# Optimization experiments

Measured on AMD Instinct MI355X. Metric: run time of the kernel, lower is better.

## Reference

```python
import jax, jax.numpy as jnp
import numpy as np

N_NODES = 50000
N_EDGES = 800000
IN_DIM = 128
HID = 64
HEADS = 4
OUT_DIM = 64
NEG_SLOPE = 0.2


def setup_inputs() -> dict:
    key = jax.random.key(0)
    ks = jax.random.split(key, 12)
    x = jax.random.normal(ks[0], (N_NODES, IN_DIM), dtype=jnp.float32)
    edge_index = jax.random.randint(ks[1], (2, N_EDGES), 0, N_NODES, dtype=jnp.int64)
    s = 0.1
    # GATConv layer 1: in_dim -> hid per head, 4 heads, concat
    W1 = jax.random.normal(ks[2], (IN_DIM, HEADS * HID), dtype=jnp.float32) * s
    a_src1 = jax.random.normal(ks[3], (HEADS, HID), dtype=jnp.float32) * s
    a_dst1 = jax.random.normal(ks[4], (HEADS, HID), dtype=jnp.float32) * s
    b1 = jnp.zeros((HEADS * HID,), dtype=jnp.float32)
    # GATConv layer 2: hid*heads -> out_dim, 1 head
    W2 = jax.random.normal(ks[5], (HEADS * HID, OUT_DIM), dtype=jnp.float32) * s
    a_src2 = jax.random.normal(ks[6], (1, OUT_DIM), dtype=jnp.float32) * s
    a_dst2 = jax.random.normal(ks[7], (1, OUT_DIM), dtype=jnp.float32) * s
    b2 = jnp.zeros((OUT_DIM,), dtype=jnp.float32)
    # final linear out_dim -> 1
    fc_w = jax.random.normal(ks[8], (OUT_DIM, 1), dtype=jnp.float32) * s
    fc_b = jnp.zeros((1,), dtype=jnp.float32)
    return {"x": x, "edge_index": edge_index, "W1": W1, "a_src1": a_src1,
            "a_dst1": a_dst1, "b1": b1, "W2": W2, "a_src2": a_src2,
            "a_dst2": a_dst2, "b2": b2, "fc_w": fc_w, "fc_b": fc_b}


def _gat_layer(x, src, dst, W, a_src, a_dst, bias, heads, out_c):
    """PyG-style GATConv: gather, edge attention, segment softmax, scatter-sum."""
    n = x.shape[0]
    h = (x @ W).reshape(n, heads, out_c)                    # [N,H,C]
    alpha_s = jnp.sum(h * a_src, axis=-1)                   # [N,H]
    alpha_d = jnp.sum(h * a_dst, axis=-1)                   # [N,H]
    e = jax.nn.leaky_relu(alpha_s[src] + alpha_d[dst], NEG_SLOPE)  # [E,H]
    # segment softmax over incoming edges of each destination node
    m = jax.ops.segment_max(e, dst, num_segments=n)         # [N,H]
    ex = jnp.exp(e - m[dst])
    den = jax.ops.segment_sum(ex, dst, num_segments=n)      # [N,H]
    alpha = ex / (den[dst] + 1e-16)                         # [E,H]
    out = jax.ops.segment_sum(alpha[:, :, None] * h[src], dst, num_segments=n)
    return out.reshape(n, heads * out_c) + bias


def reference(x, edge_index, W1, a_src1, a_dst1, b1, W2, a_src2, a_dst2, b2, fc_w, fc_b):
    n = x.shape[0]
    # GATConv default add_self_loops=True
    loop = jnp.arange(n, dtype=edge_index.dtype)
    src = jnp.concatenate([edge_index[0], loop])
    dst = jnp.concatenate([edge_index[1], loop])
    h = _gat_layer(x, src, dst, W1, a_src1, a_dst1, b1, HEADS, HID)
    h = jax.nn.elu(h)
    h = _gat_layer(h, src, dst, W2, a_src2, a_dst2, b2, 1, OUT_DIM)
    return jnp.squeeze(h @ fc_w + fc_b)                      # [N]
```

## Files before the change

kernel.cpp:

```cpp
#include <hip/hip_runtime.h>
#include <hip/hip_fp16.h>

#define N_NODES 50000
#define N_EDGES 800000
#define E_TOT   850000
#define IN_DIM  128
#define HID     64
#define HEADS   4
#define C1      256
#define OUT_DIM 64
#define NEG_SLOPE 0.2f

#define CP_NODES   32
#define CP_BLOCKS  ((N_NODES + CP_NODES - 1) / CP_NODES)
#define COUNT_BLOCKS ((E_TOT + 255) / 256)
#define NB_SCAN ((N_NODES + 255) / 256)

typedef __attribute__((ext_vector_type(8))) short v8s;
typedef __attribute__((ext_vector_type(4))) float v4f;

__device__ __forceinline__ unsigned int bf16_rne(float f) {
    unsigned int u = __float_as_uint(f);
    return (u + 0x7FFFu + ((u >> 16) & 1u)) >> 16;
}
__device__ __forceinline__ unsigned int bf16_pack2(float a, float b) {
    return bf16_rne(a) | (bf16_rne(b) << 16);
}
__device__ __forceinline__ float bf16_lo(unsigned int u) { return __uint_as_float(u << 16); }
__device__ __forceinline__ float bf16_hi(unsigned int u) { return __uint_as_float(u & 0xFFFF0000u); }

__device__ __forceinline__ unsigned int f16_pack2(float a, float b) {
    __half2 h = __floats2half2_rn(a, b);
    return *(unsigned int*)&h;
}
__device__ __forceinline__ float2 f16_unp2(unsigned int u) {
    __half2 h = *(__half2*)&u;
    return __half22float2(h);
}

__global__ __launch_bounds__(512) void prep_kernel(
    const float* __restrict__ W1, const float* __restrict__ a_src1,
    const float* __restrict__ a_dst1,
    const float* __restrict__ W2, const float* __restrict__ a_src2,
    const float* __restrict__ a_dst2, const float* __restrict__ b2,
    const float* __restrict__ fc_w, const float* __restrict__ fc_b,
    float* __restrict__ p_src, float* __restrict__ p_dst,
    float* __restrict__ v_s, float* __restrict__ v_d, float* __restrict__ v_z,
    float* __restrict__ cst, unsigned int* __restrict__ W1b)
{
    const int t = threadIdx.x;
    const int k = t >> 2, h = t & 3;
    const float* wrow = W1 + k * C1 + h * HID;
    const float* as = a_src1 + h * HID;
    const float* ad = a_dst1 + h * HID;
    float s = 0.f, d = 0.f;
    for (int c = 0; c < HID; c++) {
        float w = wrow[c];
        s = fmaf(w, as[c], s);
        d = fmaf(w, ad[c], d);
    }
    p_src[k * HEADS + h] = s;
    p_dst[k * HEADS + h] = d;

    if (t < C1) {
        const float* w2row = W2 + t * OUT_DIM;
        float vs = 0.f, vd = 0.f, vz = 0.f;
        for (int c = 0; c < OUT_DIM; c++) {
            float w = w2row[c];
            vs = fmaf(w, a_src2[c], vs);
            vd = fmaf(w, a_dst2[c], vd);
            vz = fmaf(w, fc_w[c], vz);
        }
        v_s[t] = vs; v_d[t] = vd; v_z[t] = vz;
    }
    if (t == 0) {
        float s2 = 0.f;
        for (int c = 0; c < OUT_DIM; c++) s2 = fmaf(b2[c], fc_w[c], s2);
        cst[0] = s2 + fc_b[0];
    }

    for (int idx = t; idx < 16384; idx += 512) {
        int i    = idx & 3;
        int lane = (idx >> 2) & 63;
        int kk   = (idx >> 8) & 3;
        int nt   = (idx >> 10) & 3;
        int hh   = idx >> 12;
        int k0 = kk * 32 + (lane >> 4) * 8 + i * 2;
        int c  = hh * 64 + nt * 16 + (lane & 15);
        W1b[idx] = bf16_pack2(W1[(size_t)k0 * C1 + c], W1[(size_t)(k0 + 1) * C1 + c]);
    }
}

__global__ __launch_bounds__(256) void convproj_count_kernel(
    const float* __restrict__ x, const float* __restrict__ p_src,
    const float* __restrict__ p_dst, const int* __restrict__ dst_a,
    float* __restrict__ as1, float* __restrict__ ad1,
    unsigned int* __restrict__ xb, int* __restrict__ deg,
    int* __restrict__ posE)
{
    if (blockIdx.x >= CP_BLOCKS) {
        int j = (blockIdx.x - CP_BLOCKS) * 256 + threadIdx.x;
        if (j < E_TOT) {
            int d = (j < N_EDGES) ? dst_a[j] : (j - N_EDGES);
            posE[j] = atomicAdd(&deg[d], 1);
        }
        return;
    }
    __shared__ float ps[IN_DIM * HEADS];
    __shared__ float pd[IN_DIM * HEADS];
    const int t = threadIdx.x;
    for (int i = t; i < IN_DIM * HEADS; i += 256) { ps[i] = p_src[i]; pd[i] = p_dst[i]; }
    __syncthreads();
    const int wv   = t >> 6;
    const int lane = t & 63;
    float4 p0 = *(const float4*)(ps + (lane * 2) * HEADS);
    float4 p1 = *(const float4*)(ps + (lane * 2 + 1) * HEADS);
    float4 q0 = *(const float4*)(pd + (lane * 2) * HEADS);
    float4 q1 = *(const float4*)(pd + (lane * 2 + 1) * HEADS);
    const int nodeBase = blockIdx.x * CP_NODES + wv * 8;
    #pragma unroll
    for (int i = 0; i < 8; i++) {
        const int node = nodeBase + i;
        if (node >= N_NODES) break;
        float2 xv = *(const float2*)(x + (size_t)node * IN_DIM + lane * 2);
        xb[(size_t)node * 64 + lane] = bf16_pack2(xv.x, xv.y);
        float s0 = xv.x * p0.x + xv.y * p1.x;
        float s1 = xv.x * p0.y + xv.y * p1.y;
        float s2 = xv.x * p0.z + xv.y * p1.z;
        float s3 = xv.x * p0.w + xv.y * p1.w;
        float d0 = xv.x * q0.x + xv.y * q1.x;
        float d1 = xv.x * q0.y + xv.y * q1.y;
        float d2 = xv.x * q0.z + xv.y * q1.z;
        float d3 = xv.x * q0.w + xv.y * q1.w;
        #pragma unroll
        for (int off = 32; off; off >>= 1) {
            s0 += __shfl_down(s0, off, 64); s1 += __shfl_down(s1, off, 64);
            s2 += __shfl_down(s2, off, 64); s3 += __shfl_down(s3, off, 64);
            d0 += __shfl_down(d0, off, 64); d1 += __shfl_down(d1, off, 64);
            d2 += __shfl_down(d2, off, 64); d3 += __shfl_down(d3, off, 64);
        }
        if (lane == 0) {
            float4 sv = {s0, s1, s2, s3};
            float4 dv = {d0, d1, d2, d3};
            *(float4*)(as1 + node * 4) = sv;
            *(float4*)(ad1 + node * 4) = dv;
        }
    }
}

__global__ __launch_bounds__(256) void blocksum_kernel(
    const int* __restrict__ deg, int* __restrict__ bsum)
{
    __shared__ int ps[256];
    const int t = threadIdx.x;
    int i = blockIdx.x * 256 + t;
    ps[t] = (i < N_NODES) ? deg[i] : 0;
    __syncthreads();
    for (int off = 128; off; off >>= 1) {
        if (t < off) ps[t] += ps[t + off];
        __syncthreads();
    }
    if (t == 0) bsum[blockIdx.x] = ps[0];
}

__global__ __launch_bounds__(256) void scanbsum_kernel(
    const int* __restrict__ bsum, int* __restrict__ boff)
{
    __shared__ int ps[256];
    const int t = threadIdx.x;
    ps[t] = (t < NB_SCAN) ? bsum[t] : 0;
    __syncthreads();
    for (int off = 1; off < 256; off <<= 1) {
        int u = (t >= off) ? ps[t - off] : 0;
        __syncthreads();
        ps[t] += u;
        __syncthreads();
    }
    boff[t] = (t > 0) ? ps[t - 1] : 0;
}

__global__ __launch_bounds__(256) void expand_kernel(
    const int* __restrict__ deg, const int* __restrict__ boff,
    int* __restrict__ rowptr)
{
    __shared__ int ps[256];
    const int t = threadIdx.x;
    int i = blockIdx.x * 256 + t;
    int v = (i < N_NODES) ? deg[i] : 0;
    ps[t] = v;
    __syncthreads();
    for (int off = 1; off < 256; off <<= 1) {
        int u = (t >= off) ? ps[t - off] : 0;
        __syncthreads();
        ps[t] += u;
        __syncthreads();
    }
    if (i <= N_NODES) rowptr[i] = boff[blockIdx.x] + ps[t] - v;
}

__global__ void fillw3_kernel(const int* __restrict__ src_a, const int* __restrict__ dst_a,
                              const int* __restrict__ rowptr, const int* __restrict__ posE,
                              const float* __restrict__ as1, const float* __restrict__ ad1,
                              int4* __restrict__ rec)
{
    int j = blockIdx.x * blockDim.x + threadIdx.x;
    if (j >= E_TOT) return;
    int s, d;
    if (j < N_EDGES) { s = src_a[j]; d = dst_a[j]; }
    else             { s = j - N_EDGES; d = s; }
    int slot = rowptr[d] + posE[j];
    float4 A  = *(const float4*)(as1 + s * 4);
    float4 Dv = *(const float4*)(ad1 + d * 4);
    float a0 = A.x + Dv.x, a1 = A.y + Dv.y, a2 = A.z + Dv.z, a3 = A.w + Dv.w;
    a0 = a0 > 0.f ? a0 : NEG_SLOPE * a0;
    a1 = a1 > 0.f ? a1 : NEG_SLOPE * a1;
    a2 = a2 > 0.f ? a2 : NEG_SLOPE * a2;
    a3 = a3 > 0.f ? a3 : NEG_SLOPE * a3;
    int4 r;
    r.x = s;
    r.y = (int)f16_pack2(__expf(a0), __expf(a1));
    r.z = (int)f16_pack2(__expf(a2), __expf(a3));
    r.w = 0;
    rec[slot] = r;
}

__global__ __launch_bounds__(256, 4) void agg1mlp_kernel(
    const int* __restrict__ rowptr, const int4* __restrict__ rec,
    const unsigned int* __restrict__ xb,
    const unsigned int* __restrict__ W1b, const float* __restrict__ b1,
    const float* __restrict__ v_s, const float* __restrict__ v_d,
    const float* __restrict__ v_z,
    float2* __restrict__ az, float* __restrict__ ad2)
{
    __shared__ unsigned int xsh[16 * 260];
    __shared__ float pr[4 * 16 * 3];
    const int t = threadIdx.x;
    const int nodeBase = blockIdx.x * 16;
    const int wv   = t >> 6;
    const int lane = t & 63;

    #pragma unroll 1
    for (int i = 0; i < 4; i++) {
        const int ln = wv * 4 + i;
        const int n  = nodeBase + ln;
        const int e0 = rowptr[n], e1 = rowptr[n + 1];

        float2 acc0 = {0,0}, acc1 = {0,0}, acc2 = {0,0}, acc3 = {0,0};
        float den0 = 0, den1 = 0, den2 = 0, den3 = 0;
        int e = e0;
        for (; e + 4 <= e1; e += 4) {
            int4 r0 = rec[e],     r1 = rec[e + 1];
            int4 r2 = rec[e + 2], r3 = rec[e + 3];
            unsigned int xu0 = xb[(size_t)r0.x * 64 + lane];
            unsigned int xu1 = xb[(size_t)r1.x * 64 + lane];
            unsigned int xu2 = xb[(size_t)r2.x * 64 + lane];
            unsigned int xu3 = xb[(size_t)r3.x * 64 + lane];
            float2 W0a = f16_unp2(r0.y), W0b = f16_unp2(r0.z);
            float2 W1a = f16_unp2(r1.y), W1b_ = f16_unp2(r1.z);
            float2 W2a = f16_unp2(r2.y), W2b = f16_unp2(r2.z);
            float2 W3a = f16_unp2(r3.y), W3b = f16_unp2(r3.z);
            float a0 = bf16_lo(xu0), b0 = bf16_hi(xu0);
            float a1 = bf16_lo(xu1), b1v = bf16_hi(xu1);
            float a2 = bf16_lo(xu2), b2v = bf16_hi(xu2);
            float a3 = bf16_lo(xu3), b3v = bf16_hi(xu3);
            acc0.x = fmaf(W0a.x, a0, acc0.x); acc0.y = fmaf(W0a.x, b0, acc0.y);
            acc1.x = fmaf(W0a.y, a0, acc1.x); acc1.y = fmaf(W0a.y, b0, acc1.y);
            acc2.x = fmaf(W0b.x, a0, acc2.x); acc2.y = fmaf(W0b.x, b0, acc2.y);
            acc3.x = fmaf(W0b.y, a0, acc3.x); acc3.y = fmaf(W0b.y, b0, acc3.y);
            acc0.x = fmaf(W1a.x, a1, acc0.x); acc0.y = fmaf(W1a.x, b1v, acc0.y);
            acc1.x = fmaf(W1a.y, a1, acc1.x); acc1.y = fmaf(W1a.y, b1v, acc1.y);
            acc2.x = fmaf(W1b_.x, a1, acc2.x); acc2.y = fmaf(W1b_.x, b1v, acc2.y);
            acc3.x = fmaf(W1b_.y, a1, acc3.x); acc3.y = fmaf(W1b_.y, b1v, acc3.y);
            acc0.x = fmaf(W2a.x, a2, acc0.x); acc0.y = fmaf(W2a.x, b2v, acc0.y);
            acc1.x = fmaf(W2a.y, a2, acc1.x); acc1.y = fmaf(W2a.y, b2v, acc1.y);
            acc2.x = fmaf(W2b.x, a2, acc2.x); acc2.y = fmaf(W2b.x, b2v, acc2.y);
            acc3.x = fmaf(W2b.y, a2, acc3.x); acc3.y = fmaf(W2b.y, b2v, acc3.y);
            acc0.x = fmaf(W3a.x, a3, acc0.x); acc0.y = fmaf(W3a.x, b3v, acc0.y);
            acc1.x = fmaf(W3a.y, a3, acc1.x); acc1.y = fmaf(W3a.y, b3v, acc1.y);
            acc2.x = fmaf(W3b.x, a3, acc2.x); acc2.y = fmaf(W3b.x, b3v, acc2.y);
            acc3.x = fmaf(W3b.y, a3, acc3.x); acc3.y = fmaf(W3b.y, b3v, acc3.y);
            den0 += (W0a.x + W1a.x) + (W2a.x + W3a.x);
            den1 += (W0a.y + W1a.y) + (W2a.y + W3a.y);
            den2 += (W0b.x + W1b_.x) + (W2b.x + W3b.x);
            den3 += (W0b.y + W1b_.y) + (W2b.y + W3b.y);
        }
        for (; e < e1; e++) {
            int4 r0 = rec[e];
            unsigned int xu = xb[(size_t)r0.x * 64 + lane];
            float2 Wa = f16_unp2(r0.y), Wb = f16_unp2(r0.z);
            float xa = bf16_lo(xu), xbv = bf16_hi(xu);
            acc0.x = fmaf(Wa.x, xa, acc0.x); acc0.y = fmaf(Wa.x, xbv, acc0.y);
            acc1.x = fmaf(Wa.y, xa, acc1.x); acc1.y = fmaf(Wa.y, xbv, acc1.y);
            acc2.x = fmaf(Wb.x, xa, acc2.x); acc2.y = fmaf(Wb.x, xbv, acc2.y);
            acc3.x = fmaf(Wb.y, xa, acc3.x); acc3.y = fmaf(Wb.y, xbv, acc3.y);
            den0 += Wa.x; den1 += Wa.y; den2 += Wb.x; den3 += Wb.y;
        }
        float i0 = 1.f / (den0 + 1e-16f), i1 = 1.f / (den1 + 1e-16f);
        float i2 = 1.f / (den2 + 1e-16f), i3 = 1.f / (den3 + 1e-16f);
        unsigned int* o = xsh + ln * 260 + lane;
        o[0 * 64] = bf16_pack2(acc0.x * i0, acc0.y * i0);
        o[1 * 64] = bf16_pack2(acc1.x * i1, acc1.y * i1);
        o[2 * 64] = bf16_pack2(acc2.x * i2, acc2.y * i2);
        o[3 * 64] = bf16_pack2(acc3.x * i3, acc3.y * i3);
    }
    __syncthreads();

    {
        const int h = wv;
        const int m = lane & 15, quad = lane >> 4;
        const unsigned int* abase = xsh + m * 260 + h * 64 + quad * 4;
        v8s af0 = *(const v8s*)(abase + 0);
        v8s af1 = *(const v8s*)(abase + 16);
        v8s af2 = *(const v8s*)(abase + 32);
        v8s af3 = *(const v8s*)(abase + 48);

        float Sr[4] = {0,0,0,0}, Dr[4] = {0,0,0,0}, Zr[4] = {0,0,0,0};
        #pragma unroll
        for (int nt = 0; nt < 4; nt++) {
            const unsigned int* bbase = W1b + (size_t)(h * 16 + nt * 4) * 256 + lane * 4;
            v4f acc = {0.f, 0.f, 0.f, 0.f};
            acc = __builtin_amdgcn_mfma_f32_16x16x32_bf16(af0, *(const v8s*)(bbase + 0 * 256), acc, 0, 0, 0);
            acc = __builtin_amdgcn_mfma_f32_16x16x32_bf16(af1, *(const v8s*)(bbase + 1 * 256), acc, 0, 0, 0);
            acc = __builtin_amdgcn_mfma_f32_16x16x32_bf16(af2, *(const v8s*)(bbase + 2 * 256), acc, 0, 0, 0);
            acc = __builtin_amdgcn_mfma_f32_16x16x32_bf16(af3, *(const v8s*)(bbase + 3 * 256), acc, 0, 0, 0);
            const int c = h * 64 + nt * 16 + m;
            float bb = b1[c], vsc = v_s[c], vdc = v_d[c], vzc = v_z[c];
            #pragma unroll
            for (int r = 0; r < 4; r++) {
                float o = acc[r] + bb;
                o = o > 0.f ? o : __expf(o) - 1.f;
                Sr[r] = fmaf(o, vsc, Sr[r]);
                Dr[r] = fmaf(o, vdc, Dr[r]);
                Zr[r] = fmaf(o, vzc, Zr[r]);
            }
        }
        #pragma unroll
        for (int off = 8; off; off >>= 1) {
            #pragma unroll
            for (int r = 0; r < 4; r++) {
                Sr[r] += __shfl_down(Sr[r], off, 16);
                Dr[r] += __shfl_down(Dr[r], off, 16);
                Zr[r] += __shfl_down(Zr[r], off, 16);
            }
        }
        if (m == 0) {
            #pragma unroll
            for (int r = 0; r < 4; r++) {
                const int row = quad * 4 + r;
                pr[(h * 16 + row) * 3 + 0] = Sr[r];
                pr[(h * 16 + row) * 3 + 1] = Dr[r];
                pr[(h * 16 + row) * 3 + 2] = Zr[r];
            }
        }
    }
    __syncthreads();

    if (t < 16) {
        float s = 0.f, d = 0.f, z = 0.f;
        #pragma unroll
        for (int w = 0; w < 4; w++) {
            s += pr[(w * 16 + t) * 3 + 0];
            d += pr[(w * 16 + t) * 3 + 1];
            z += pr[(w * 16 + t) * 3 + 2];
        }
        const int node = nodeBase + t;
        float2 azv = {s, z};
        az[node]  = azv;
        ad2[node] = d;
    }
}

__global__ __launch_bounds__(256) void agg2z_kernel(
    const int* __restrict__ rowptr, const int4* __restrict__ rec,
    const float2* __restrict__ az, const float* __restrict__ ad2,
    const float* __restrict__ cst, float* __restrict__ out)
{
    int gid  = blockIdx.x * blockDim.x + threadIdx.x;
    int n    = gid >> 3;
    int sl   = threadIdx.x & 7;
    if (n >= N_NODES) return;
    const float adh = ad2[n];
    const int e0 = rowptr[n], e1 = rowptr[n + 1];

    float acc = 0.f, den = 0.f;
    for (int e = e0 + sl; e < e1; e += 8) {
        int s = rec[e].x;
        float2 v = az[s];
        float a = v.x + adh;
        a = a > 0.f ? a : NEG_SLOPE * a;
        float w = __expf(a);
        acc = fmaf(w, v.y, acc);
        den += w;
    }
    #pragma unroll
    for (int off = 4; off; off >>= 1) {
        acc += __shfl_down(acc, off, 8);
        den += __shfl_down(den, off, 8);
    }
    if (sl == 0) out[n] = acc / (den + 1e-16f) + cst[0];
}

extern "C" void kernel_launch(void* const* d_in, const int* in_sizes, int n_in,
                              void* d_out, int out_size, void* d_ws, size_t ws_size,
                              hipStream_t stream)
{
    const float* x      = (const float*)d_in[0];
    const int*   ei     = (const int*)d_in[1];
    const float* W1     = (const float*)d_in[2];
    const float* a_src1 = (const float*)d_in[3];
    const float* a_dst1 = (const float*)d_in[4];
    const float* b1     = (const float*)d_in[5];
    const float* W2     = (const float*)d_in[6];
    const float* a_src2 = (const float*)d_in[7];
    const float* a_dst2 = (const float*)d_in[8];
    const float* b2     = (const float*)d_in[9];
    const float* fc_w   = (const float*)d_in[10];
    const float* fc_b   = (const float*)d_in[11];
    float* out = (float*)d_out;

    const int* srcA = ei;
    const int* dstA = ei + N_EDGES;

    float* ws = (float*)d_ws;
    size_t off = 0;
    unsigned int* xb    = (unsigned int*)(ws + off); off += (size_t)N_NODES * 64;
    int4* rec      = (int4*)(ws + off); off += (size_t)E_TOT * 4 + 256;
    int* posE      = (int*)(ws + off); off += E_TOT + 256;
    float* as1     = ws + off; off += (size_t)N_NODES * HEADS;
    float* ad1     = ws + off; off += (size_t)N_NODES * HEADS;
    float2* az     = (float2*)(ws + off); off += (size_t)N_NODES * 2;
    float* ad2     = ws + off; off += N_NODES;
    float* p_src   = ws + off; off += IN_DIM * HEADS;
    float* p_dst   = ws + off; off += IN_DIM * HEADS;
    float* v_s     = ws + off; off += C1;
    float* v_d     = ws + off; off += C1;
    float* v_z     = ws + off; off += C1;
    float* cst     = ws + off; off += 2;
    unsigned int* W1b = (unsigned int*)(ws + off); off += 16384;
    int* rowptr    = (int*)(ws + off); off += N_NODES + 1 + 256;
    int* bsum      = (int*)(ws + off); off += 256;
    int* boff      = (int*)(ws + off); off += 256;
    int* deg       = (int*)(ws + off); off += N_NODES;
    hipMemsetAsync(deg, 0, N_NODES * sizeof(int), stream);

    prep_kernel<<<1, 512, 0, stream>>>(W1, a_src1, a_dst1, W2, a_src2, a_dst2,
                                       b2, fc_w, fc_b, p_src, p_dst, v_s, v_d, v_z, cst, W1b);

    convproj_count_kernel<<<CP_BLOCKS + COUNT_BLOCKS, 256, 0, stream>>>(
        x, p_src, p_dst, dstA, as1, ad1, xb, deg, posE);

    blocksum_kernel<<<NB_SCAN, 256, 0, stream>>>(deg, bsum);
    scanbsum_kernel<<<1, 256, 0, stream>>>(bsum, boff);
    expand_kernel<<<NB_SCAN, 256, 0, stream>>>(deg, boff, rowptr);
    fillw3_kernel<<<COUNT_BLOCKS, 256, 0, stream>>>(srcA, dstA, rowptr, posE,
                                                    as1, ad1, rec);

    agg1mlp_kernel<<<N_NODES / 16, 256, 0, stream>>>(rowptr, rec, xb, W1b, b1,
                                                     v_s, v_d, v_z, az, ad2);

    agg2z_kernel<<<(N_NODES * 8 + 255) / 256, 256, 0, stream>>>(rowptr, rec, az, ad2, cst, out);
}
```

Measured before the change: 247.6 us.

## Double agg1mlp block to 512 threads and prefetch edge records

The fused aggregation+MLP kernel now uses 8 waves per 16-node block, so each wave aggregates 2 nodes instead of 4. In the MFMA stage each wave handles half of one head's output tiles, and the partial-sum reduction covers 8 waves. The edge loop also loads the next group of 4 edge records before doing the current group's FMAs, to hide record-load latency. The intent is more parallelism and memory-level overlap in the gather-bound phase, at the cost of more registers per iteration and a larger block that may limit occupancy.

```diff
diff --git a/kernel.cpp b/kernel.cpp
--- a/kernel.cpp
+++ b/kernel.cpp
@@ -224,7 +224,7 @@
     rec[slot] = r;
 }
 
-__global__ __launch_bounds__(256, 4) void agg1mlp_kernel(
+__global__ __launch_bounds__(512, 8) void agg1mlp_kernel(
     const int* __restrict__ rowptr, const int4* __restrict__ rec,
     const unsigned int* __restrict__ xb,
     const unsigned int* __restrict__ W1b, const float* __restrict__ b1,
@@ -233,32 +233,40 @@
     float2* __restrict__ az, float* __restrict__ ad2)
 {
     __shared__ unsigned int xsh[16 * 260];
-    __shared__ float pr[4 * 16 * 3];
+    __shared__ float pr[8 * 16 * 3];
     const int t = threadIdx.x;
     const int nodeBase = blockIdx.x * 16;
     const int wv   = t >> 6;
     const int lane = t & 63;
 
     #pragma unroll 1
-    for (int i = 0; i < 4; i++) {
-        const int ln = wv * 4 + i;
+    for (int i = 0; i < 2; i++) {
+        const int ln = wv * 2 + i;
         const int n  = nodeBase + ln;
         const int e0 = rowptr[n], e1 = rowptr[n + 1];
 
         float2 acc0 = {0,0}, acc1 = {0,0}, acc2 = {0,0}, acc3 = {0,0};
         float den0 = 0, den1 = 0, den2 = 0, den3 = 0;
         int e = e0;
-        for (; e + 4 <= e1; e += 4) {
-            int4 r0 = rec[e],     r1 = rec[e + 1];
-            int4 r2 = rec[e + 2], r3 = rec[e + 3];
-            unsigned int xu0 = xb[(size_t)r0.x * 64 + lane];
-            unsigned int xu1 = xb[(size_t)r1.x * 64 + lane];
-            unsigned int xu2 = xb[(size_t)r2.x * 64 + lane];
-            unsigned int xu3 = xb[(size_t)r3.x * 64 + lane];
-            float2 W0a = f16_unp2(r0.y), W0b = f16_unp2(r0.z);
-            float2 W1a = f16_unp2(r1.y), W1b_ = f16_unp2(r1.z);
-            float2 W2a = f16_unp2(r2.y), W2b = f16_unp2(r2.z);
-            float2 W3a = f16_unp2(r3.y), W3b = f16_unp2(r3.z);
+        int4 R0, R1, R2, R3;
+        if (e + 4 <= e1) {
+            R0 = rec[e]; R1 = rec[e + 1]; R2 = rec[e + 2]; R3 = rec[e + 3];
+        }
+        while (e + 4 <= e1) {
+            unsigned int xu0 = xb[(size_t)R0.x * 64 + lane];
+            unsigned int xu1 = xb[(size_t)R1.x * 64 + lane];
+            unsigned int xu2 = xb[(size_t)R2.x * 64 + lane];
+            unsigned int xu3 = xb[(size_t)R3.x * 64 + lane];
+            unsigned int wy0 = R0.y, wz0 = R0.z, wy1 = R1.y, wz1 = R1.z;
+            unsigned int wy2 = R2.y, wz2 = R2.z, wy3 = R3.y, wz3 = R3.z;
+            e += 4;
+            if (e + 4 <= e1) {
+                R0 = rec[e]; R1 = rec[e + 1]; R2 = rec[e + 2]; R3 = rec[e + 3];
+            }
+            float2 W0a = f16_unp2(wy0), W0b = f16_unp2(wz0);
+            float2 W1a = f16_unp2(wy1), W1b_ = f16_unp2(wz1);
+            float2 W2a = f16_unp2(wy2), W2b = f16_unp2(wz2);
+            float2 W3a = f16_unp2(wy3), W3b = f16_unp2(wz3);
             float a0 = bf16_lo(xu0), b0 = bf16_hi(xu0);
             float a1 = bf16_lo(xu1), b1v = bf16_hi(xu1);
             float a2 = bf16_lo(xu2), b2v = bf16_hi(xu2);
@@ -306,7 +314,8 @@
     __syncthreads();
 
     {
-        const int h = wv;
+        const int h = wv >> 1;
+        const int ntb = (wv & 1) * 2;
         const int m = lane & 15, quad = lane >> 4;
         const unsigned int* abase = xsh + m * 260 + h * 64 + quad * 4;
         v8s af0 = *(const v8s*)(abase + 0);
@@ -316,7 +325,8 @@
 
         float Sr[4] = {0,0,0,0}, Dr[4] = {0,0,0,0}, Zr[4] = {0,0,0,0};
         #pragma unroll
-        for (int nt = 0; nt < 4; nt++) {
+        for (int j = 0; j < 2; j++) {
+            const int nt = ntb + j;
             const unsigned int* bbase = W1b + (size_t)(h * 16 + nt * 4) * 256 + lane * 4;
             v4f acc = {0.f, 0.f, 0.f, 0.f};
             acc = __builtin_amdgcn_mfma_f32_16x16x32_bf16(af0, *(const v8s*)(bbase + 0 * 256), acc, 0, 0, 0);
@@ -347,9 +357,9 @@
             #pragma unroll
             for (int r = 0; r < 4; r++) {
                 const int row = quad * 4 + r;
-                pr[(h * 16 + row) * 3 + 0] = Sr[r];
-                pr[(h * 16 + row) * 3 + 1] = Dr[r];
-                pr[(h * 16 + row) * 3 + 2] = Zr[r];
+                pr[(wv * 16 + row) * 3 + 0] = Sr[r];
+                pr[(wv * 16 + row) * 3 + 1] = Dr[r];
+                pr[(wv * 16 + row) * 3 + 2] = Zr[r];
             }
         }
     }
@@ -358,7 +368,7 @@
     if (t < 16) {
         float s = 0.f, d = 0.f, z = 0.f;
         #pragma unroll
-        for (int w = 0; w < 4; w++) {
+        for (int w = 0; w < 8; w++) {
             s += pr[(w * 16 + t) * 3 + 0];
             d += pr[(w * 16 + t) * 3 + 1];
             z += pr[(w * 16 + t) * 3 + 2];
@@ -455,7 +465,7 @@
     fillw3_kernel<<<COUNT_BLOCKS, 256, 0, stream>>>(srcA, dstA, rowptr, posE,
                                                     as1, ad1, rec);
 
-    agg1mlp_kernel<<<N_NODES / 16, 256, 0, stream>>>(rowptr, rec, xb, W1b, b1,
+    agg1mlp_kernel<<<N_NODES / 16, 512, 0, stream>>>(rowptr, rec, xb, W1b, b1,
                                                      v_s, v_d, v_z, az, ad2);
 
     agg2z_kernel<<<(N_NODES * 8 + 255) / 256, 256, 0, stream>>>(rowptr, rec, az, ad2, cst, out);
```

Result: slower. 255.8 us (+3.3%).
